# Kernel tuning notes

Measured on AMD Instinct MI355X. Metric: run time of the kernel, lower is better.

The kernel has to match this reference:

```python
import jax, jax.numpy as jnp
import numpy as np

N_HEADS = 16

def setup_inputs() -> dict:
    key = jax.random.key(0)
    k1, k2, k3, k4 = jax.random.split(key, 4)
    B, N, E = 4, 2048, 1024
    x = jax.random.normal(k1, (B, N, E), dtype=jnp.float32)
    s = 1.0 / np.sqrt(E)
    Wq = jax.random.normal(k2, (E, E), dtype=jnp.float32) * s
    Wk = jax.random.normal(k3, (E, E), dtype=jnp.float32) * s
    Wv = jax.random.normal(k4, (E, E), dtype=jnp.float32) * s
    return {"x": x, "Wq": Wq, "Wk": Wk, "Wv": Wv}

def reference(x, Wq, Wk, Wv):
    # first_block=False -> PositionalEncoding is identity: encoded_vectors = x
    B, N, E = x.shape
    H = N_HEADS
    D = E // H
    norm = np.sqrt(D).astype(np.float32)
    # torch nn.Linear(bias=False): y = x @ W.T
    q = (x @ Wq.T).reshape(B, N, H, D).transpose(0, 2, 1, 3)  # [B,H,N,D]
    k = (x @ Wk.T).reshape(B, N, H, D).transpose(0, 2, 1, 3)
    v = (x @ Wv.T).reshape(B, N, H, D).transpose(0, 2, 1, 3)
    scores = jnp.einsum('bhnd,bhmd->bhnm', q, k) / norm  # [B,H,N,N]
    attn = jax.nn.softmax(scores, axis=-1)
    # original einsum 'stuu, stuv -> stuv': diagonal of attn scales values
    diag = jnp.diagonal(attn, axis1=-2, axis2=-1)  # [B,H,N]
    av = diag[..., None] * v  # [B,H,N,D]
    av = av.transpose(0, 2, 1, 3).reshape(B, N, E)
    return (av, x)
```

## Files before the change

kernel.cpp:

```cpp
#include <hip/hip_runtime.h>
#include <hip/hip_bf16.h>
#include <stdint.h>

typedef __attribute__((ext_vector_type(8))) short short8;
typedef __attribute__((ext_vector_type(4))) float f32x4;

#define BATCH 4
#define SEQ   2048
#define EMB   1024
#define HEADS 16
#define DHEAD 64
#define MROWS (BATCH * SEQ)

#define QSCALE 0.18033688011112042f

__device__ inline unsigned short f2bf(float f) {
    unsigned int u = __float_as_uint(f);
    unsigned int r = (u + 0x7fffu + ((u >> 16) & 1u)) >> 16;
    return (unsigned short)r;
}

__device__ __forceinline__ void gl_lds16(const short* g, short* l) {
    __builtin_amdgcn_global_load_lds(
        (const __attribute__((address_space(1))) void*)g,
        (__attribute__((address_space(3))) void*)l, 16, 0, 0);
}

__global__ __launch_bounds__(256) void pack_x(const float* __restrict__ src,
                                              unsigned short* __restrict__ dst,
                                              float* __restrict__ pass) {
    int i = (blockIdx.x * 256 + threadIdx.x) * 8;
    const float4* s = reinterpret_cast<const float4*>(src + i);
    float4 f0 = s[0];
    float4 f1 = s[1];
    union { unsigned short u[8]; short8 v; } o;
    o.u[0] = f2bf(f0.x); o.u[1] = f2bf(f0.y); o.u[2] = f2bf(f0.z); o.u[3] = f2bf(f0.w);
    o.u[4] = f2bf(f1.x); o.u[5] = f2bf(f1.y); o.u[6] = f2bf(f1.z); o.u[7] = f2bf(f1.w);
    *reinterpret_cast<short8*>(dst + i) = o.v;
    float4* p = reinterpret_cast<float4*>(pass + i);
    p[0] = f0;
    p[1] = f1;
}

__global__ __launch_bounds__(256) void pack_w3(const float* __restrict__ wq,
                                               const float* __restrict__ wk,
                                               const float* __restrict__ wv,
                                               unsigned short* __restrict__ dq,
                                               unsigned short* __restrict__ dk,
                                               unsigned short* __restrict__ dv) {
    const float* src = blockIdx.y == 0 ? wq : blockIdx.y == 1 ? wk : wv;
    unsigned short* dst = blockIdx.y == 0 ? dq : blockIdx.y == 1 ? dk : dv;
    int i = (blockIdx.x * 256 + threadIdx.x) * 8;
    const float4* s = reinterpret_cast<const float4*>(src + i);
    float4 f0 = s[0];
    float4 f1 = s[1];
    union { unsigned short u[8]; short8 v; } o;
    o.u[0] = f2bf(f0.x); o.u[1] = f2bf(f0.y); o.u[2] = f2bf(f0.z); o.u[3] = f2bf(f0.w);
    o.u[4] = f2bf(f1.x); o.u[5] = f2bf(f1.y); o.u[6] = f2bf(f1.z); o.u[7] = f2bf(f1.w);
    *reinterpret_cast<short8*>(dst + i) = o.v;
}

template <int MODE>
__global__ __launch_bounds__(256) void gemm_bt(const short* __restrict__ A,
                                               const short* __restrict__ Bm,
                                               unsigned short* __restrict__ Cb,
                                               float* __restrict__ out,
                                               const float* __restrict__ dgp,
                                               float escale) {
    constexpr int K = EMB;
    constexpr int N = EMB;
    __shared__ short As[128 * 32];
    __shared__ short Bs[128 * 32];
    const int m0 = blockIdx.x * 128;
    const int n0 = blockIdx.y * 128;
    const int t = threadIdx.x;
    const int lane = t & 63;
    const int w = t >> 6;
    const int wr = w >> 1, wc = w & 1;

    f32x4 acc[4][4] = {};

    const short* gA = A + (size_t)(m0 + (t >> 2)) * K + (t & 3) * 8;
    const short* gB = Bm + (size_t)(n0 + (t >> 2)) * K + (t & 3) * 8;
    short* lA0 = As + w * 512;
    short* lA1 = As + 2048 + w * 512;
    short* lB0 = Bs + w * 512;
    short* lB1 = Bs + 2048 + w * 512;

    const int kq = (lane >> 4) * 8;
    const int fr = lane & 15;

    for (int k0 = 0; k0 < K; k0 += 32) {
        gl_lds16(gA + k0, lA0);
        gl_lds16(gA + 64 * K + k0, lA1);
        gl_lds16(gB + k0, lB0);
        gl_lds16(gB + 64 * K + k0, lB1);
        __syncthreads();

        short8 a[4], b[4];
#pragma unroll
        for (int i = 0; i < 4; i++)
            a[i] = *(const short8*)&As[(wr * 64 + i * 16 + fr) * 32 + kq];
#pragma unroll
        for (int j = 0; j < 4; j++)
            b[j] = *(const short8*)&Bs[(wc * 64 + j * 16 + fr) * 32 + kq];
#pragma unroll
        for (int i = 0; i < 4; i++)
#pragma unroll
            for (int j = 0; j < 4; j++)
                acc[i][j] = __builtin_amdgcn_mfma_f32_16x16x32_bf16(a[i], b[j], acc[i][j], 0, 0, 0);
        __syncthreads();
    }

    const int gr_base = m0 + wr * 64 + (lane >> 4) * 4;
    const int gc_base = n0 + wc * 64 + fr;
#pragma unroll
    for (int i = 0; i < 4; i++) {
#pragma unroll
        for (int j = 0; j < 4; j++) {
            const int col = gc_base + j * 16;
#pragma unroll
            for (int r = 0; r < 4; r++) {
                const int grow = gr_base + i * 16 + r;
                const int bb = grow >> 11;
                const int nn = grow & 2047;
                const int hh = col >> 6;
                if (MODE == 0) {
                    const int dd = col & 63;
                    Cb[(((size_t)((bb << 4) + hh) * SEQ + nn) << 6) + dd] =
                        f2bf(acc[i][j][r] * escale);
                } else {
                    const float d = dgp[((bb << 4) + hh) * SEQ + nn];
                    out[(size_t)grow * N + col] = acc[i][j][r] * d;
                }
            }
        }
    }
}

#define KT 128

__global__ __launch_bounds__(512) void diag_kernel(const short* __restrict__ Qh,
                                                   const short* __restrict__ Kh,
                                                   float* __restrict__ dgp) {
    const int bh = blockIdx.x >> 4;
    const int qt = blockIdx.x & 15;
    __shared__ short Ks[2][KT][64];

    const int t = threadIdx.x;
    const int lane = t & 63;
    const int w = t >> 6;
    const int rl = lane & 15;
    const int g = lane >> 4;
    const int kq = g * 8;

    const short* Kbh = Kh + (size_t)bh * SEQ * DHEAD;
    const short* Qbh = Qh + (size_t)bh * SEQ * DHEAD;

    const int qrow = qt * 128 + w * 16 + rl;
    const short8 a0 = *(const short8*)(Qbh + qrow * DHEAD + kq);
    const short8 a1 = *(const short8*)(Qbh + qrow * DHEAD + kq + 32);

    const int r0 = t >> 3;
    const int c0 = t & 7;
    const int cs = (c0 ^ (r0 & 7)) * 8;

    *(short8*)&Ks[0][r0][cs]      = *(const short8*)&Kbh[r0 * DHEAD + c0 * 8];
    *(short8*)&Ks[0][r0 + 64][cs] = *(const short8*)&Kbh[(r0 + 64) * DHEAD + c0 * 8];
    __syncthreads();

    const int blk0 = (g ^ (lane & 7)) * 8;
    const int blk1 = ((g + 4) ^ (lane & 7)) * 8;

    float ssum[4] = {0.f, 0.f, 0.f, 0.f};
    float sdiag = 0.f;
    int buf = 0;

    for (int kt = 0; kt < SEQ / KT; ++kt) {
        short8 p0, p1;
        if (kt < SEQ / KT - 1) {
            const short* src = Kbh + (kt + 1) * KT * DHEAD;
            p0 = *(const short8*)&src[r0 * DHEAD + c0 * 8];
            p1 = *(const short8*)&src[(r0 + 64) * DHEAD + c0 * 8];
        }
#pragma unroll
        for (int sub = 0; sub < 8; ++sub) {
            const int row = sub * 16 + rl;
            const short8 b0 = *(const short8*)&Ks[buf][row][blk0];
            const short8 b1 = *(const short8*)&Ks[buf][row][blk1];
            f32x4 c = {};
            c = __builtin_amdgcn_mfma_f32_16x16x32_bf16(a0, b0, c, 0, 0, 0);
            c = __builtin_amdgcn_mfma_f32_16x16x32_bf16(a1, b1, c, 0, 0, 0);
            if (kt == qt && sub == w) {
                const int r = rl - g * 4;
                if (r >= 0 && r < 4) sdiag = c[r];
            }
#pragma unroll
            for (int r = 0; r < 4; ++r)
                ssum[r] += __builtin_amdgcn_exp2f(c[r]);
        }
        if (kt < SEQ / KT - 1) {
            __syncthreads();
            *(short8*)&Ks[buf ^ 1][r0][cs]      = p0;
            *(short8*)&Ks[buf ^ 1][r0 + 64][cs] = p1;
            __syncthreads();
        }
        buf ^= 1;
    }

#pragma unroll
    for (int r = 0; r < 4; r++) {
        float v = ssum[r];
        v += __shfl_xor(v, 1);
        v += __shfl_xor(v, 2);
        v += __shfl_xor(v, 4);
        v += __shfl_xor(v, 8);
        ssum[r] = v;
    }

    const int j = rl;
    const int r = j - g * 4;
    if (r >= 0 && r < 4) {
        const float dg = __builtin_amdgcn_exp2f(sdiag) / ssum[r];
        dgp[bh * SEQ + qt * 128 + w * 16 + j] = dg;
    }
}

extern "C" void kernel_launch(void* const* d_in, const int* in_sizes, int n_in,
                              void* d_out, int out_size, void* d_ws, size_t ws_size,
                              hipStream_t stream) {
    const float* x  = (const float*)d_in[0];
    const float* Wq = (const float*)d_in[1];
    const float* Wk = (const float*)d_in[2];
    const float* Wv = (const float*)d_in[3];
    float* out = (float*)d_out;
    char* ws = (char*)d_ws;

    const size_t xb_off  = 0;
    const size_t wq_off  = xb_off + (size_t)MROWS * EMB * 2;
    const size_t wk_off  = wq_off + (size_t)EMB * EMB * 2;
    const size_t wv_off  = wk_off + (size_t)EMB * EMB * 2;
    const size_t q_off   = wv_off + (size_t)EMB * EMB * 2;
    const size_t k_off   = q_off + (size_t)MROWS * EMB * 2;
    const size_t dg_off  = k_off + (size_t)MROWS * EMB * 2;

    short* xb  = (short*)(ws + xb_off);
    short* wqb = (short*)(ws + wq_off);
    short* wkb = (short*)(ws + wk_off);
    short* wvb = (short*)(ws + wv_off);
    short* Qh  = (short*)(ws + q_off);
    short* Kh  = (short*)(ws + k_off);
    float* dgp = (float*)(ws + dg_off);

    const int nx = MROWS * EMB;
    const int nw = EMB * EMB;

    pack_x<<<nx / 2048, 256, 0, stream>>>(x, (unsigned short*)xb,
                                          out + (size_t)MROWS * EMB);
    pack_w3<<<dim3(nw / 2048, 3), 256, 0, stream>>>(Wq, Wk, Wv,
                                                    (unsigned short*)wqb,
                                                    (unsigned short*)wkb,
                                                    (unsigned short*)wvb);

    dim3 grid(MROWS / 128, EMB / 128);
    gemm_bt<0><<<grid, 256, 0, stream>>>(xb, wqb, (unsigned short*)Qh, nullptr, nullptr, QSCALE);
    gemm_bt<0><<<grid, 256, 0, stream>>>(xb, wkb, (unsigned short*)Kh, nullptr, nullptr, 1.0f);

    diag_kernel<<<BATCH * HEADS * (SEQ / 128), 512, 0, stream>>>(Qh, Kh, dgp);

    gemm_bt<1><<<grid, 256, 0, stream>>>(xb, wvb, nullptr, out, dgp, 1.0f);
}
```

Baseline: 154.2 us.

## Fuse Q/K projections into one GEMM and register-block diag kernel over queries

Result: slower. 164.3 us (+6.6%).

```diff
diff --git a/kernel.cpp b/kernel.cpp
--- a/kernel.cpp
+++ b/kernel.cpp
@@ -65,10 +65,8 @@
                                                const short* __restrict__ Bm,
                                                unsigned short* __restrict__ Cb,
                                                float* __restrict__ out,
-                                               const float* __restrict__ dgp,
-                                               float escale) {
+                                               const float* __restrict__ dgp) {
     constexpr int K = EMB;
-    constexpr int N = EMB;
     __shared__ short As[128 * 32];
     __shared__ short Bs[128 * 32];
     const int m0 = blockIdx.x * 128;
@@ -124,14 +122,18 @@
                 const int grow = gr_base + i * 16 + r;
                 const int bb = grow >> 11;
                 const int nn = grow & 2047;
-                const int hh = col >> 6;
                 if (MODE == 0) {
-                    const int dd = col & 63;
-                    Cb[(((size_t)((bb << 4) + hh) * SEQ + nn) << 6) + dd] =
-                        f2bf(acc[i][j][r] * escale);
+                    const int sel = col >> 10;
+                    const int cc = col & 1023;
+                    const int hh = cc >> 6;
+                    const int dd = cc & 63;
+                    const float sc = sel ? 1.0f : QSCALE;
+                    Cb[(((size_t)((sel << 6) + (bb << 4) + hh) * SEQ + nn) << 6) + dd] =
+                        f2bf(acc[i][j][r] * sc);
                 } else {
+                    const int hh = col >> 6;
                     const float d = dgp[((bb << 4) + hh) * SEQ + nn];
-                    out[(size_t)grow * N + col] = acc[i][j][r] * d;
+                    out[(size_t)grow * EMB + col] = acc[i][j][r] * d;
                 }
             }
         }
@@ -140,11 +142,11 @@
 
 #define KT 128
 
-__global__ __launch_bounds__(512) void diag_kernel(const short* __restrict__ Qh,
+__global__ __launch_bounds__(256) void diag_kernel(const short* __restrict__ Qh,
                                                    const short* __restrict__ Kh,
                                                    float* __restrict__ dgp) {
-    const int bh = blockIdx.x >> 4;
-    const int qt = blockIdx.x & 15;
+    const int bh = blockIdx.x >> 3;
+    const int qt = blockIdx.x & 7;
     __shared__ short Ks[2][KT][64];
 
     const int t = threadIdx.x;
@@ -157,72 +159,101 @@
     const short* Kbh = Kh + (size_t)bh * SEQ * DHEAD;
     const short* Qbh = Qh + (size_t)bh * SEQ * DHEAD;
 
-    const int qrow = qt * 128 + w * 16 + rl;
-    const short8 a0 = *(const short8*)(Qbh + qrow * DHEAD + kq);
-    const short8 a1 = *(const short8*)(Qbh + qrow * DHEAD + kq + 32);
-
-    const int r0 = t >> 3;
-    const int c0 = t & 7;
-    const int cs = (c0 ^ (r0 & 7)) * 8;
-
-    *(short8*)&Ks[0][r0][cs]      = *(const short8*)&Kbh[r0 * DHEAD + c0 * 8];
-    *(short8*)&Ks[0][r0 + 64][cs] = *(const short8*)&Kbh[(r0 + 64) * DHEAD + c0 * 8];
+    const int qbase = qt * 256 + w * 64;
+    short8 a0[4], a1[4];
+#pragma unroll
+    for (int i = 0; i < 4; i++) {
+        const int qrow = qbase + i * 16 + rl;
+        a0[i] = *(const short8*)(Qbh + qrow * DHEAD + kq);
+        a1[i] = *(const short8*)(Qbh + qrow * DHEAD + kq + 32);
+    }
+
+    float sdiag[4];
+    const int rr = rl - g * 4;
+#pragma unroll
+    for (int i = 0; i < 4; i++) {
+        const int krow = qbase + i * 16 + rl;
+        const short8 b0d = *(const short8*)(Kbh + krow * DHEAD + kq);
+        const short8 b1d = *(const short8*)(Kbh + krow * DHEAD + kq + 32);
+        f32x4 cd = {};
+        cd = __builtin_amdgcn_mfma_f32_16x16x32_bf16(a0[i], b0d, cd, 0, 0, 0);
+        cd = __builtin_amdgcn_mfma_f32_16x16x32_bf16(a1[i], b1d, cd, 0, 0, 0);
+        sdiag[i] = (rr >= 0 && rr < 4) ? cd[rr] : 0.f;
+    }
+
+    const int sr = t >> 1;
+    const int sh = (t & 1) * 4;
+
+#pragma unroll
+    for (int j = 0; j < 4; j++) {
+        const int cb = sh + j;
+        const int cs = (cb ^ (sr & 7)) * 8;
+        *(short8*)&Ks[0][sr][cs] = *(const short8*)&Kbh[sr * DHEAD + cb * 8];
+    }
     __syncthreads();
 
     const int blk0 = (g ^ (lane & 7)) * 8;
     const int blk1 = ((g + 4) ^ (lane & 7)) * 8;
 
-    float ssum[4] = {0.f, 0.f, 0.f, 0.f};
-    float sdiag = 0.f;
+    float ssum[4][4] = {};
     int buf = 0;
 
     for (int kt = 0; kt < SEQ / KT; ++kt) {
-        short8 p0, p1;
+        short8 p[4];
         if (kt < SEQ / KT - 1) {
             const short* src = Kbh + (kt + 1) * KT * DHEAD;
-            p0 = *(const short8*)&src[r0 * DHEAD + c0 * 8];
-            p1 = *(const short8*)&src[(r0 + 64) * DHEAD + c0 * 8];
+#pragma unroll
+            for (int j = 0; j < 4; j++)
+                p[j] = *(const short8*)&src[sr * DHEAD + (sh + j) * 8];
         }
 #pragma unroll
         for (int sub = 0; sub < 8; ++sub) {
             const int row = sub * 16 + rl;
             const short8 b0 = *(const short8*)&Ks[buf][row][blk0];
             const short8 b1 = *(const short8*)&Ks[buf][row][blk1];
-            f32x4 c = {};
-            c = __builtin_amdgcn_mfma_f32_16x16x32_bf16(a0, b0, c, 0, 0, 0);
-            c = __builtin_amdgcn_mfma_f32_16x16x32_bf16(a1, b1, c, 0, 0, 0);
-            if (kt == qt && sub == w) {
-                const int r = rl - g * 4;
-                if (r >= 0 && r < 4) sdiag = c[r];
+            f32x4 c[4];
+#pragma unroll
+            for (int i = 0; i < 4; i++) {
+                c[i] = __builtin_amdgcn_mfma_f32_16x16x32_bf16(a0[i], b0, f32x4{}, 0, 0, 0);
+                c[i] = __builtin_amdgcn_mfma_f32_16x16x32_bf16(a1[i], b1, c[i], 0, 0, 0);
             }
 #pragma unroll
-            for (int r = 0; r < 4; ++r)
-                ssum[r] += __builtin_amdgcn_exp2f(c[r]);
+            for (int i = 0; i < 4; i++)
+#pragma unroll
+                for (int r = 0; r < 4; ++r)
+                    ssum[i][r] += __builtin_amdgcn_exp2f(c[i][r]);
         }
         if (kt < SEQ / KT - 1) {
             __syncthreads();
-            *(short8*)&Ks[buf ^ 1][r0][cs]      = p0;
-            *(short8*)&Ks[buf ^ 1][r0 + 64][cs] = p1;
+#pragma unroll
+            for (int j = 0; j < 4; j++) {
+                const int cb = sh + j;
+                const int cs = (cb ^ (sr & 7)) * 8;
+                *(short8*)&Ks[buf ^ 1][sr][cs] = p[j];
+            }
             __syncthreads();
         }
         buf ^= 1;
     }
 
 #pragma unroll
-    for (int r = 0; r < 4; r++) {
-        float v = ssum[r];
-        v += __shfl_xor(v, 1);
-        v += __shfl_xor(v, 2);
-        v += __shfl_xor(v, 4);
-        v += __shfl_xor(v, 8);
-        ssum[r] = v;
-    }
-
-    const int j = rl;
-    const int r = j - g * 4;
-    if (r >= 0 && r < 4) {
-        const float dg = __builtin_amdgcn_exp2f(sdiag) / ssum[r];
-        dgp[bh * SEQ + qt * 128 + w * 16 + j] = dg;
+    for (int i = 0; i < 4; i++)
+#pragma unroll
+        for (int r = 0; r < 4; r++) {
+            float v = ssum[i][r];
+            v += __shfl_xor(v, 1);
+            v += __shfl_xor(v, 2);
+            v += __shfl_xor(v, 4);
+            v += __shfl_xor(v, 8);
+            ssum[i][r] = v;
+        }
+
+    if (rr >= 0 && rr < 4) {
+#pragma unroll
+        for (int i = 0; i < 4; i++) {
+            const float dg = __builtin_amdgcn_exp2f(sdiag[i]) / ssum[i][rr];
+            dgp[bh * SEQ + qbase + i * 16 + rl] = dg;
+        }
     }
 }
 
@@ -262,11 +293,11 @@
                                                     (unsigned short*)wkb,
                                                     (unsigned short*)wvb);
 
-    dim3 grid(MROWS / 128, EMB / 128);
-    gemm_bt<0><<<grid, 256, 0, stream>>>(xb, wqb, (unsigned short*)Qh, nullptr, nullptr, QSCALE);
-    gemm_bt<0><<<grid, 256, 0, stream>>>(xb, wkb, (unsigned short*)Kh, nullptr, nullptr, 1.0f);
-
-    diag_kernel<<<BATCH * HEADS * (SEQ / 128), 512, 0, stream>>>(Qh, Kh, dgp);
-
-    gemm_bt<1><<<grid, 256, 0, stream>>>(xb, wvb, nullptr, out, dgp, 1.0f);
-}
+    gemm_bt<0><<<dim3(MROWS / 128, 2048 / 128), 256, 0, stream>>>(
+        xb, wqb, (unsigned short*)Qh, nullptr, nullptr);
+
+    diag_kernel<<<BATCH * HEADS * (SEQ / 256), 256, 0, stream>>>(Qh, Kh, dgp);
+
+    gemm_bt<1><<<dim3(MROWS / 128, EMB / 128), 256, 0, stream>>>(
+        xb, wvb, nullptr, out, dgp);
+}
```
